# Kernel tuning notes

Hardware: AMD Instinct MI355X
Metric: run time of the kernel (lower is better)

The kernel has to match this reference:

```python
import jax, jax.numpy as jnp
import numpy as np

CLAMP = 1e20
EPS_LN = 1e-5
EPS_DEN = 1e-5


def setup_inputs() -> dict:
    key = jax.random.key(0)
    ks = jax.random.split(key, 8)
    B, T, Fin, D = 4, 2048, 512, 128
    s = 1.0 / np.sqrt(Fin)
    s2 = 1.0 / np.sqrt(D)
    return {
        "history": jax.random.normal(ks[0], (B, T, Fin), dtype=jnp.float32),
        "S0": jnp.zeros((B, 1, D, D), dtype=jnp.float32),
        "Z0": jnp.zeros((B, 1, D), dtype=jnp.float32),
        "Wk": jax.random.normal(ks[1], (Fin, D), dtype=jnp.float32) * s,
        "Wq": jax.random.normal(ks[2], (Fin, D), dtype=jnp.float32) * s,
        "Wv": jax.random.normal(ks[3], (Fin, D), dtype=jnp.float32) * s,
        "ln_g": jnp.ones((Fin,), dtype=jnp.float32),
        "ln_b": jnp.zeros((Fin,), dtype=jnp.float32),
        "w1": jax.random.normal(ks[4], (D, D), dtype=jnp.float32) * s2,
        "b1": jnp.zeros((D,), dtype=jnp.float32),
        "w2": jax.random.normal(ks[5], (D, D), dtype=jnp.float32) * s2,
        "b2": jnp.zeros((D,), dtype=jnp.float32),
        "sc_w": jax.random.normal(ks[6], (Fin, D), dtype=jnp.float32) * s,
        "sc_b": jnp.zeros((D,), dtype=jnp.float32),
    }


def reference(history, S0, Z0, Wk, Wq, Wv, ln_g, ln_b, w1, b1, w2, b2, sc_w, sc_b):
    # LayerNorm over feature dim
    mu = jnp.mean(history, axis=-1, keepdims=True)
    var = jnp.mean((history - mu) ** 2, axis=-1, keepdims=True)
    x = (history - mu) / jnp.sqrt(var + EPS_LN) * ln_g + ln_b  # [B,T,Fin]

    phi = lambda z: jax.nn.elu(z) + 1.0
    K = phi(x @ Wk)  # [B,T,D]
    Q = phi(x @ Wq)  # [B,T,D]
    V = x @ Wv       # [B,T,D]

    # S_t = clamp(cumsum_t(K_t outer V_t)) + S0  -> [B,T,D,D]
    KV = jnp.einsum('bti,btj->btij', K, V)
    S = jnp.clip(jnp.cumsum(KV, axis=1), -CLAMP, CLAMP) + S0
    # Z_t = clamp(cumsum_t(K_t)) + Z0 -> [B,T,D]
    Z = jnp.clip(jnp.cumsum(K, axis=1), -CLAMP, CLAMP) + Z0

    numerator = jnp.einsum('bti,btil->btl', Q, S)            # [B,T,D]
    denominator = jnp.einsum('bti,bti->bt', Q, Z)[..., None] + EPS_DEN
    out = numerator / denominator

    # feed-forward: Linear->ReLU->Linear->ReLU
    out = jax.nn.relu(jax.nn.relu(out @ w1 + b1) @ w2 + b2)
    # residual shortcut from normalized input
    out = out + x @ sc_w + sc_b
    return out, S, Z
```

## Files before the change

kernel.cpp:

```cpp
#include <hip/hip_runtime.h>
#include <math.h>

#define BB 4
#define TT 2048
#define FIN 512
#define DD 128
#define NC 64
#define CT 32
#define ROWS (BB*TT)
#define CLAMP_V 1e20f
#define EPS_LN_ 1e-5f
#define EPS_DEN_ 1e-5f

__global__ __launch_bounds__(256) void k0_stats(const float* __restrict__ h,
                                                float* __restrict__ stats) {
  int wv = threadIdx.x >> 6, lane = threadIdx.x & 63;
  int row = blockIdx.x * 4 + wv;
  const float* hr = h + (size_t)row * FIN;
  float s = 0.f, sq = 0.f;
#pragma unroll
  for (int j = 0; j < FIN / 64; ++j) {
    float v = hr[lane + 64 * j];
    s += v; sq += v * v;
  }
#pragma unroll
  for (int m = 32; m >= 1; m >>= 1) {
    s += __shfl_xor(s, m);
    sq += __shfl_xor(sq, m);
  }
  if (lane == 0) {
    float mu = s * (1.f / FIN);
    float var = sq * (1.f / FIN) - mu * mu;
    stats[row * 2] = mu;
    stats[row * 2 + 1] = rsqrtf(var + EPS_LN_);
  }
}

__global__ __launch_bounds__(256) void k1_lngemm(
    const float* __restrict__ h, const float* __restrict__ stats,
    const float* __restrict__ ln_g, const float* __restrict__ ln_b,
    const float* __restrict__ Wk, const float* __restrict__ Wq,
    const float* __restrict__ Wv, const float* __restrict__ Wsc,
    float* __restrict__ Kb, float* __restrict__ Qb,
    float* __restrict__ Vb, float* __restrict__ SCb) {
  __shared__ float As[32 * 129];
  __shared__ float Bs[32 * 128];
  __shared__ float stS[256];
  __shared__ float lnS[2 * FIN];
  int tid = threadIdx.x;
  int row0 = blockIdx.x * 128;
  int wsel = blockIdx.y;
  const float* W = (wsel == 0) ? Wk : (wsel == 1) ? Wq : (wsel == 2) ? Wv : Wsc;
  float* Ob = (wsel == 0) ? Kb : (wsel == 1) ? Qb : (wsel == 2) ? Vb : SCb;
  int ty = tid >> 4, tx = tid & 15;
  if (tid < 128) {
    stS[tid * 2] = stats[(row0 + tid) * 2];
    stS[tid * 2 + 1] = stats[(row0 + tid) * 2 + 1];
  }
  for (int j = tid; j < FIN; j += 256) {
    lnS[j] = ln_g[j];
    lnS[FIN + j] = ln_b[j];
  }
  float acc[8][8];
#pragma unroll
  for (int i = 0; i < 8; ++i)
#pragma unroll
    for (int j = 0; j < 8; ++j) acc[i][j] = 0.f;

  int ar = tid >> 5, af = tid & 31;
  int bk = tid >> 7, bn = tid & 127;
  float ra[16], rb[16];
#pragma unroll
  for (int j = 0; j < 16; ++j) {
    ra[j] = h[(size_t)(row0 + ar + 8 * j) * FIN + af];
    rb[j] = W[(size_t)(bk + 2 * j) * DD + bn];
  }
  __syncthreads();
#pragma unroll
  for (int j = 0; j < 16; ++j) {
    int r = ar + 8 * j;
    float mu = stS[r * 2], rs = stS[r * 2 + 1];
    As[af * 129 + r] = (ra[j] - mu) * rs * lnS[af] + lnS[FIN + af];
    Bs[(bk + 2 * j) * 128 + bn] = rb[j];
  }
  __syncthreads();

  for (int ks = 0; ks < FIN; ks += 32) {
    bool more = (ks + 32) < FIN;
    if (more) {
#pragma unroll
      for (int j = 0; j < 16; ++j) {
        ra[j] = h[(size_t)(row0 + ar + 8 * j) * FIN + ks + 32 + af];
        rb[j] = W[(size_t)(ks + 32 + bk + 2 * j) * DD + bn];
      }
    }
#pragma unroll
    for (int k = 0; k < 32; ++k) {
      float a[8], bv[8];
#pragma unroll
      for (int i = 0; i < 8; ++i) a[i] = As[k * 129 + ty * 8 + i];
#pragma unroll
      for (int j = 0; j < 8; ++j) bv[j] = Bs[k * 128 + tx * 8 + j];
#pragma unroll
      for (int i = 0; i < 8; ++i)
#pragma unroll
        for (int j = 0; j < 8; ++j) acc[i][j] = fmaf(a[i], bv[j], acc[i][j]);
    }
    __syncthreads();
    if (more) {
#pragma unroll
      for (int j = 0; j < 16; ++j) {
        int r = ar + 8 * j;
        float mu = stS[r * 2], rs = stS[r * 2 + 1];
        As[af * 129 + r] = (ra[j] - mu) * rs * lnS[ks + 32 + af] + lnS[FIN + ks + 32 + af];
        Bs[(bk + 2 * j) * 128 + bn] = rb[j];
      }
      __syncthreads();
    }
  }
  bool phi = (wsel < 2);
#pragma unroll
  for (int i = 0; i < 8; ++i) {
    int row = row0 + ty * 8 + i;
#pragma unroll
    for (int j = 0; j < 8; ++j) {
      float z = acc[i][j];
      if (phi) z = (z > 0.f) ? (z + 1.f) : expf(z);
      Ob[(size_t)row * DD + tx * 8 + j] = z;
    }
  }
}

__global__ __launch_bounds__(256) void k2_chunksum(const float* __restrict__ Kb,
                                                   const float* __restrict__ Vb,
                                                   float* __restrict__ kvsum,
                                                   float* __restrict__ ksum) {
  int bc = blockIdx.x;
  int b = bc >> 6, c = bc & 63;
  __shared__ float Kc[CT * 128];
  __shared__ float Vc[CT * 128];
  int tid = threadIdx.x;
  size_t base = (size_t)(b * TT + c * CT) * 128;
#pragma unroll
  for (int j = 0; j < 16; ++j) {
    int idx = tid + 256 * j;
    Kc[idx] = Kb[base + idx];
    Vc[idx] = Vb[base + idx];
  }
  __syncthreads();
  int ti = tid >> 4, tl = tid & 15;
  int i0 = ti * 8, l0 = tl * 8;
  float acc[8][8];
#pragma unroll
  for (int i = 0; i < 8; ++i)
#pragma unroll
    for (int j = 0; j < 8; ++j) acc[i][j] = 0.f;
  for (int t = 0; t < CT; ++t) {
    float kk[8], vv[8];
#pragma unroll
    for (int i = 0; i < 8; ++i) kk[i] = Kc[t * 128 + i0 + i];
#pragma unroll
    for (int j = 0; j < 8; ++j) vv[j] = Vc[t * 128 + l0 + j];
#pragma unroll
    for (int i = 0; i < 8; ++i)
#pragma unroll
      for (int j = 0; j < 8; ++j) acc[i][j] = fmaf(kk[i], vv[j], acc[i][j]);
  }
  size_t ob = (size_t)bc * 16384;
#pragma unroll
  for (int i = 0; i < 8; ++i)
#pragma unroll
    for (int j = 0; j < 8; ++j)
      kvsum[ob + (size_t)(i0 + i) * 128 + l0 + j] = acc[i][j];
  if (tid < 128) {
    float s = 0.f;
    for (int t = 0; t < CT; ++t) s += Kc[t * 128 + tid];
    ksum[bc * 128 + tid] = s;
  }
}

__global__ __launch_bounds__(256) void k3_prefix(float* __restrict__ kvsum,
                                                 float* __restrict__ ksum) {
  int gid = blockIdx.x * 256 + threadIdx.x;
  int b = gid >> 14, rem = gid & 16383;
  size_t base = (size_t)b * NC * 16384 + rem;
  float run = 0.f;
  for (int c = 0; c < NC; ++c) {
    size_t idx = base + (size_t)c * 16384;
    float t = kvsum[idx];
    kvsum[idx] = run;
    run += t;
  }
  if (gid < BB * 128) {
    int b2 = gid >> 7, i = gid & 127;
    float r2 = 0.f;
    for (int c = 0; c < NC; ++c) {
      int idx = (b2 * NC + c) * 128 + i;
      float t = ksum[idx];
      ksum[idx] = r2;
      r2 += t;
    }
  }
}

__global__ __launch_bounds__(128) void k4_zden(const float* __restrict__ Kb,
                                               const float* __restrict__ Qb,
                                               const float* __restrict__ ksum,
                                               const float* __restrict__ Z0,
                                               float* __restrict__ Zout,
                                               float* __restrict__ den) {
  __shared__ float denp[2 * CT];
  int bx = blockIdx.x;
  int b = bx >> 6, c = bx & 63;
  int i = threadIdx.x;
  int wv = i >> 6, lane = i & 63;
  float z = ksum[(b * NC + c) * 128 + i];
  float z0 = Z0[b * 128 + i];
  size_t rb = (size_t)(b * TT + c * CT) * 128;
  float kcur = Kb[rb + i], qcur = Qb[rb + i];
  for (int t = 0; t < CT; ++t) {
    float kn = 0.f, qn = 0.f;
    if (t + 1 < CT) {
      kn = Kb[rb + (size_t)(t + 1) * 128 + i];
      qn = Qb[rb + (size_t)(t + 1) * 128 + i];
    }
    z += kcur;
    float zc = fminf(fmaxf(z, -CLAMP_V), CLAMP_V) + z0;
    Zout[rb + (size_t)t * 128 + i] = zc;
    float p = qcur * zc;
#pragma unroll
    for (int m = 32; m >= 1; m >>= 1) p += __shfl_xor(p, m);
    if (lane == 0) denp[wv * CT + t] = p;
    kcur = kn; qcur = qn;
  }
  __syncthreads();
  if (i < CT) den[b * TT + c * CT + i] = denp[i] + denp[CT + i] + EPS_DEN_;
}

__global__ __launch_bounds__(256) void k6_main(
    const float* __restrict__ Kb, const float* __restrict__ Qb,
    const float* __restrict__ Vb, const float* __restrict__ kvpref,
    const float* __restrict__ S0, const float* __restrict__ den,
    float* __restrict__ Sout, float* __restrict__ Aout) {
  __shared__ float KQ[CT * 128 * 2];
  __shared__ float NA[4 * CT * 64];
  int tid = threadIdx.x;
  int lhalf = blockIdx.x, c = blockIdx.y, b = blockIdx.z;
  int w = tid >> 6, lane = tid & 63;
  int i0 = w * 32;
  int l = lhalf * 64 + lane;
  int row0r = b * TT + c * CT;
  size_t rowbase = (size_t)row0r * 128;
#pragma unroll
  for (int j = 0; j < 16; ++j) {
    int idx = tid + 256 * j;
    KQ[idx * 2] = Kb[rowbase + idx];
    KQ[idx * 2 + 1] = Qb[rowbase + idx];
  }
  float s[32], s0[32];
  int bc = b * NC + c;
#pragma unroll
  for (int ii = 0; ii < 32; ++ii) {
    s[ii] = kvpref[(size_t)bc * 16384 + (size_t)(i0 + ii) * 128 + l];
    s0[ii] = S0[((size_t)b * 128 + i0 + ii) * 128 + l];
  }
  __syncthreads();
  float v = Vb[rowbase + l];
  for (int t = 0; t < CT; ++t) {
    float vn = 0.f;
    if (t + 1 < CT) vn = Vb[rowbase + (size_t)(t + 1) * 128 + l];
    float num = 0.f;
    size_t sb = ((size_t)(row0r + t) * 128 + i0) * 128 + l;
#pragma unroll
    for (int ii = 0; ii < 32; ++ii) {
      float2 kq = *(const float2*)&KQ[(t * 128 + i0 + ii) * 2];
      s[ii] = fmaf(kq.x, v, s[ii]);
      float sc = fminf(fmaxf(s[ii], -CLAMP_V), CLAMP_V) + s0[ii];
      __builtin_nontemporal_store(sc, &Sout[sb + (size_t)ii * 128]);
      num = fmaf(kq.y, sc, num);
    }
    NA[(w * CT + t) * 64 + lane] = num;
    v = vn;
  }
  __syncthreads();
#pragma unroll
  for (int j = 0; j < 8; ++j) {
    int idx = tid + 256 * j;
    int t = idx >> 6, ll = idx & 63;
    int row = row0r + t;
    float sum = NA[idx] + NA[CT * 64 + idx] + NA[2 * CT * 64 + idx] +
                NA[3 * CT * 64 + idx];
    Aout[(size_t)row * 128 + lhalf * 64 + ll] = sum / den[row];
  }
}

__global__ __launch_bounds__(256) void k7_ff(
    const float* __restrict__ A,
    const float* __restrict__ w1, const float* __restrict__ b1,
    const float* __restrict__ w2, const float* __restrict__ b2,
    const float* __restrict__ SCb, const float* __restrict__ sc_b,
    float* __restrict__ out) {
  __shared__ float a[32 * 128];
  __shared__ float h1[32 * 128];
  int tid = threadIdx.x;
  int row0 = blockIdx.x * 32;
#pragma unroll
  for (int j = 0; j < 16; ++j) {
    int idx = tid + 256 * j;
    a[idx] = A[(size_t)(row0 + (idx >> 7)) * 128 + (idx & 127)];
  }
  __syncthreads();
  int l = tid & 127, half = tid >> 7;
  for (int rc = 0; rc < 2; ++rc) {
    int r0 = half * 16 + rc * 8;
    float acc[8];
#pragma unroll
    for (int rr = 0; rr < 8; ++rr) acc[rr] = b1[l];
    for (int k = 0; k < 128; ++k) {
      float wv = w1[k * 128 + l];
#pragma unroll
      for (int rr = 0; rr < 8; ++rr) acc[rr] = fmaf(a[(r0 + rr) * 128 + k], wv, acc[rr]);
    }
#pragma unroll
    for (int rr = 0; rr < 8; ++rr) h1[(r0 + rr) * 128 + l] = fmaxf(acc[rr], 0.f);
  }
  __syncthreads();
  for (int rc = 0; rc < 2; ++rc) {
    int r0 = half * 16 + rc * 8;
    float acc[8];
#pragma unroll
    for (int rr = 0; rr < 8; ++rr) acc[rr] = b2[l];
    for (int k = 0; k < 128; ++k) {
      float wv = w2[k * 128 + l];
#pragma unroll
      for (int rr = 0; rr < 8; ++rr) acc[rr] = fmaf(h1[(r0 + rr) * 128 + k], wv, acc[rr]);
    }
#pragma unroll
    for (int rr = 0; rr < 8; ++rr) {
      int row = row0 + r0 + rr;
      out[(size_t)row * 128 + l] =
          fmaxf(acc[rr], 0.f) + SCb[(size_t)row * 128 + l] + sc_b[l];
    }
  }
}

extern "C" void kernel_launch(void* const* d_in, const int* in_sizes, int n_in,
                              void* d_out, int out_size, void* d_ws, size_t ws_size,
                              hipStream_t stream) {
  const float* history = (const float*)d_in[0];
  const float* S0   = (const float*)d_in[1];
  const float* Z0   = (const float*)d_in[2];
  const float* Wk   = (const float*)d_in[3];
  const float* Wq   = (const float*)d_in[4];
  const float* Wv   = (const float*)d_in[5];
  const float* ln_g = (const float*)d_in[6];
  const float* ln_b = (const float*)d_in[7];
  const float* w1   = (const float*)d_in[8];
  const float* b1   = (const float*)d_in[9];
  const float* w2   = (const float*)d_in[10];
  const float* b2   = (const float*)d_in[11];
  const float* sc_w = (const float*)d_in[12];
  const float* sc_b = (const float*)d_in[13];

  float* out  = (float*)d_out;
  float* Sout = out + (size_t)ROWS * DD;
  float* Zout = Sout + (size_t)ROWS * DD * DD;

  float* ws = (float*)d_ws;
  float* stats = ws;
  float* Kb    = stats + 16384;
  float* Qb    = Kb + (size_t)ROWS * DD;
  float* Vb    = Qb + (size_t)ROWS * DD;
  float* SCb   = Vb + (size_t)ROWS * DD;
  float* kvsum = SCb + (size_t)ROWS * DD;
  float* ksum  = kvsum + (size_t)BB * NC * 16384;
  float* A     = ksum + (size_t)BB * NC * 128;
  float* den   = A + (size_t)ROWS * DD;

  k0_stats<<<ROWS / 4, 256, 0, stream>>>(history, stats);
  k1_lngemm<<<dim3(ROWS / 128, 4), 256, 0, stream>>>(history, stats, ln_g, ln_b,
                                                     Wk, Wq, Wv, sc_w,
                                                     Kb, Qb, Vb, SCb);
  k2_chunksum<<<BB * NC, 256, 0, stream>>>(Kb, Vb, kvsum, ksum);
  k3_prefix<<<(BB * DD * DD) / 256, 256, 0, stream>>>(kvsum, ksum);
  k4_zden<<<BB * NC, 128, 0, stream>>>(Kb, Qb, ksum, Z0, Zout, den);
  k6_main<<<dim3(2, NC, BB), 256, 0, stream>>>(Kb, Qb, Vb, kvsum, S0, den, Sout, A);
  k7_ff<<<ROWS / 32, 256, 0, stream>>>(A, w1, b1, w2, b2, SCb, sc_b, out);
}
```

Before: 739.3 us.

## Vectorize global loads and stores with float4 across kernels and retile FF

Converts scalar global loads and stores to float4 in the stats, LN-GEMM, chunk-sum, main and feed-forward kernels. It batches the prefix-scan loads in groups of eight and uses a nontemporal store for Z. The k6 K/Q interleaved shared buffer is split into separate arrays. The FF kernel is retiled to 4x4 per-thread outputs with vectorized weight loads. The goal is fewer memory instructions and better coalescing. The dominant cost is likely the S output store, which this leaves unchanged, so the overall effect may be small.

```diff
diff --git a/kernel.cpp b/kernel.cpp
--- a/kernel.cpp
+++ b/kernel.cpp
@@ -16,12 +16,13 @@
                                                 float* __restrict__ stats) {
   int wv = threadIdx.x >> 6, lane = threadIdx.x & 63;
   int row = blockIdx.x * 4 + wv;
-  const float* hr = h + (size_t)row * FIN;
+  const float4* hr = (const float4*)(h + (size_t)row * FIN);
   float s = 0.f, sq = 0.f;
 #pragma unroll
-  for (int j = 0; j < FIN / 64; ++j) {
-    float v = hr[lane + 64 * j];
-    s += v; sq += v * v;
+  for (int j = 0; j < 2; ++j) {
+    float4 v = hr[lane + 64 * j];
+    s += v.x + v.y + v.z + v.w;
+    sq += v.x * v.x + v.y * v.y + v.z * v.z + v.w * v.w;
   }
 #pragma unroll
   for (int m = 32; m >= 1; m >>= 1) {
@@ -67,21 +68,26 @@
 #pragma unroll
     for (int j = 0; j < 8; ++j) acc[i][j] = 0.f;
 
-  int ar = tid >> 5, af = tid & 31;
-  int bk = tid >> 7, bn = tid & 127;
-  float ra[16], rb[16];
-#pragma unroll
-  for (int j = 0; j < 16; ++j) {
-    ra[j] = h[(size_t)(row0 + ar + 8 * j) * FIN + af];
-    rb[j] = W[(size_t)(bk + 2 * j) * DD + bn];
-  }
-  __syncthreads();
-#pragma unroll
-  for (int j = 0; j < 16; ++j) {
-    int r = ar + 8 * j;
+  int ar = tid >> 3;
+  int af = (tid & 7) * 4;
+  int bk = tid >> 5;
+  int bn = (tid & 31) * 4;
+  float4 ra[4], rb[4];
+#pragma unroll
+  for (int p = 0; p < 4; ++p) {
+    ra[p] = *(const float4*)&h[(size_t)(row0 + ar + 32 * p) * FIN + af];
+    rb[p] = *(const float4*)&W[(size_t)(bk + 8 * p) * DD + bn];
+  }
+  __syncthreads();
+#pragma unroll
+  for (int p = 0; p < 4; ++p) {
+    int r = ar + 32 * p;
     float mu = stS[r * 2], rs = stS[r * 2 + 1];
-    As[af * 129 + r] = (ra[j] - mu) * rs * lnS[af] + lnS[FIN + af];
-    Bs[(bk + 2 * j) * 128 + bn] = rb[j];
+    As[(af + 0) * 129 + r] = (ra[p].x - mu) * rs * lnS[af + 0] + lnS[FIN + af + 0];
+    As[(af + 1) * 129 + r] = (ra[p].y - mu) * rs * lnS[af + 1] + lnS[FIN + af + 1];
+    As[(af + 2) * 129 + r] = (ra[p].z - mu) * rs * lnS[af + 2] + lnS[FIN + af + 2];
+    As[(af + 3) * 129 + r] = (ra[p].w - mu) * rs * lnS[af + 3] + lnS[FIN + af + 3];
+    *(float4*)&Bs[(bk + 8 * p) * 128 + bn] = rb[p];
   }
   __syncthreads();
 
@@ -89,9 +95,9 @@
     bool more = (ks + 32) < FIN;
     if (more) {
 #pragma unroll
-      for (int j = 0; j < 16; ++j) {
-        ra[j] = h[(size_t)(row0 + ar + 8 * j) * FIN + ks + 32 + af];
-        rb[j] = W[(size_t)(ks + 32 + bk + 2 * j) * DD + bn];
+      for (int p = 0; p < 4; ++p) {
+        ra[p] = *(const float4*)&h[(size_t)(row0 + ar + 32 * p) * FIN + ks + 32 + af];
+        rb[p] = *(const float4*)&W[(size_t)(ks + 32 + bk + 8 * p) * DD + bn];
       }
     }
 #pragma unroll
@@ -109,11 +115,15 @@
     __syncthreads();
     if (more) {
 #pragma unroll
-      for (int j = 0; j < 16; ++j) {
-        int r = ar + 8 * j;
+      for (int p = 0; p < 4; ++p) {
+        int r = ar + 32 * p;
         float mu = stS[r * 2], rs = stS[r * 2 + 1];
-        As[af * 129 + r] = (ra[j] - mu) * rs * lnS[ks + 32 + af] + lnS[FIN + ks + 32 + af];
-        Bs[(bk + 2 * j) * 128 + bn] = rb[j];
+        int f = ks + 32 + af;
+        As[(af + 0) * 129 + r] = (ra[p].x - mu) * rs * lnS[f + 0] + lnS[FIN + f + 0];
+        As[(af + 1) * 129 + r] = (ra[p].y - mu) * rs * lnS[f + 1] + lnS[FIN + f + 1];
+        As[(af + 2) * 129 + r] = (ra[p].z - mu) * rs * lnS[f + 2] + lnS[FIN + f + 2];
+        As[(af + 3) * 129 + r] = (ra[p].w - mu) * rs * lnS[f + 3] + lnS[FIN + f + 3];
+        *(float4*)&Bs[(bk + 8 * p) * 128 + bn] = rb[p];
       }
       __syncthreads();
     }
@@ -122,12 +132,16 @@
 #pragma unroll
   for (int i = 0; i < 8; ++i) {
     int row = row0 + ty * 8 + i;
-#pragma unroll
-    for (int j = 0; j < 8; ++j) {
-      float z = acc[i][j];
-      if (phi) z = (z > 0.f) ? (z + 1.f) : expf(z);
-      Ob[(size_t)row * DD + tx * 8 + j] = z;
-    }
+    float4 o0, o1;
+    float* z = &acc[i][0];
+    if (phi) {
+#pragma unroll
+      for (int j = 0; j < 8; ++j) z[j] = (z[j] > 0.f) ? (z[j] + 1.f) : expf(z[j]);
+    }
+    o0.x = z[0]; o0.y = z[1]; o0.z = z[2]; o0.w = z[3];
+    o1.x = z[4]; o1.y = z[5]; o1.z = z[6]; o1.w = z[7];
+    *(float4*)&Ob[(size_t)row * DD + tx * 8] = o0;
+    *(float4*)&Ob[(size_t)row * DD + tx * 8 + 4] = o1;
   }
 }
 
@@ -142,10 +156,10 @@
   int tid = threadIdx.x;
   size_t base = (size_t)(b * TT + c * CT) * 128;
 #pragma unroll
-  for (int j = 0; j < 16; ++j) {
-    int idx = tid + 256 * j;
-    Kc[idx] = Kb[base + idx];
-    Vc[idx] = Vb[base + idx];
+  for (int j = 0; j < 4; ++j) {
+    int i4 = tid + 256 * j;
+    *(float4*)&Kc[i4 * 4] = *(const float4*)&Kb[base + (size_t)i4 * 4];
+    *(float4*)&Vc[i4 * 4] = *(const float4*)&Vb[base + (size_t)i4 * 4];
   }
   __syncthreads();
   int ti = tid >> 4, tl = tid & 15;
@@ -170,8 +184,9 @@
 #pragma unroll
   for (int i = 0; i < 8; ++i)
 #pragma unroll
-    for (int j = 0; j < 8; ++j)
-      kvsum[ob + (size_t)(i0 + i) * 128 + l0 + j] = acc[i][j];
+    for (int j = 0; j < 8; j += 4)
+      *(float4*)&kvsum[ob + (size_t)(i0 + i) * 128 + l0 + j] =
+          make_float4(acc[i][j], acc[i][j + 1], acc[i][j + 2], acc[i][j + 3]);
   if (tid < 128) {
     float s = 0.f;
     for (int t = 0; t < CT; ++t) s += Kc[t * 128 + tid];
@@ -185,20 +200,28 @@
   int b = gid >> 14, rem = gid & 16383;
   size_t base = (size_t)b * NC * 16384 + rem;
   float run = 0.f;
-  for (int c = 0; c < NC; ++c) {
-    size_t idx = base + (size_t)c * 16384;
-    float t = kvsum[idx];
-    kvsum[idx] = run;
-    run += t;
+  for (int g = 0; g < NC; g += 8) {
+    float v[8];
+#pragma unroll
+    for (int j = 0; j < 8; ++j) v[j] = kvsum[base + (size_t)(g + j) * 16384];
+#pragma unroll
+    for (int j = 0; j < 8; ++j) {
+      kvsum[base + (size_t)(g + j) * 16384] = run;
+      run += v[j];
+    }
   }
   if (gid < BB * 128) {
     int b2 = gid >> 7, i = gid & 127;
     float r2 = 0.f;
-    for (int c = 0; c < NC; ++c) {
-      int idx = (b2 * NC + c) * 128 + i;
-      float t = ksum[idx];
-      ksum[idx] = r2;
-      r2 += t;
+    for (int g = 0; g < NC; g += 8) {
+      float v[8];
+#pragma unroll
+      for (int j = 0; j < 8; ++j) v[j] = ksum[(b2 * NC + g + j) * 128 + i];
+#pragma unroll
+      for (int j = 0; j < 8; ++j) {
+        ksum[(b2 * NC + g + j) * 128 + i] = r2;
+        r2 += v[j];
+      }
     }
   }
 }
@@ -226,7 +249,7 @@
     }
     z += kcur;
     float zc = fminf(fmaxf(z, -CLAMP_V), CLAMP_V) + z0;
-    Zout[rb + (size_t)t * 128 + i] = zc;
+    __builtin_nontemporal_store(zc, &Zout[rb + (size_t)t * 128 + i]);
     float p = qcur * zc;
 #pragma unroll
     for (int m = 32; m >= 1; m >>= 1) p += __shfl_xor(p, m);
@@ -242,7 +265,8 @@
     const float* __restrict__ Vb, const float* __restrict__ kvpref,
     const float* __restrict__ S0, const float* __restrict__ den,
     float* __restrict__ Sout, float* __restrict__ Aout) {
-  __shared__ float KQ[CT * 128 * 2];
+  __shared__ float Ks[CT * 128];
+  __shared__ float Qs[CT * 128];
   __shared__ float NA[4 * CT * 64];
   int tid = threadIdx.x;
   int lhalf = blockIdx.x, c = blockIdx.y, b = blockIdx.z;
@@ -252,10 +276,10 @@
   int row0r = b * TT + c * CT;
   size_t rowbase = (size_t)row0r * 128;
 #pragma unroll
-  for (int j = 0; j < 16; ++j) {
-    int idx = tid + 256 * j;
-    KQ[idx * 2] = Kb[rowbase + idx];
-    KQ[idx * 2 + 1] = Qb[rowbase + idx];
+  for (int j = 0; j < 4; ++j) {
+    int i4 = tid + 256 * j;
+    *(float4*)&Ks[i4 * 4] = *(const float4*)&Kb[rowbase + (size_t)i4 * 4];
+    *(float4*)&Qs[i4 * 4] = *(const float4*)&Qb[rowbase + (size_t)i4 * 4];
   }
   float s[32], s0[32];
   int bc = b * NC + c;
@@ -273,11 +297,12 @@
     size_t sb = ((size_t)(row0r + t) * 128 + i0) * 128 + l;
 #pragma unroll
     for (int ii = 0; ii < 32; ++ii) {
-      float2 kq = *(const float2*)&KQ[(t * 128 + i0 + ii) * 2];
-      s[ii] = fmaf(kq.x, v, s[ii]);
+      float kk = Ks[t * 128 + i0 + ii];
+      float qq = Qs[t * 128 + i0 + ii];
+      s[ii] = fmaf(kk, v, s[ii]);
       float sc = fminf(fmaxf(s[ii], -CLAMP_V), CLAMP_V) + s0[ii];
       __builtin_nontemporal_store(sc, &Sout[sb + (size_t)ii * 128]);
-      num = fmaf(kq.y, sc, num);
+      num = fmaf(qq, sc, num);
     }
     NA[(w * CT + t) * 64 + lane] = num;
     v = vn;
@@ -305,42 +330,69 @@
   int tid = threadIdx.x;
   int row0 = blockIdx.x * 32;
 #pragma unroll
-  for (int j = 0; j < 16; ++j) {
-    int idx = tid + 256 * j;
-    a[idx] = A[(size_t)(row0 + (idx >> 7)) * 128 + (idx & 127)];
-  }
-  __syncthreads();
-  int l = tid & 127, half = tid >> 7;
-  for (int rc = 0; rc < 2; ++rc) {
-    int r0 = half * 16 + rc * 8;
-    float acc[8];
-#pragma unroll
-    for (int rr = 0; rr < 8; ++rr) acc[rr] = b1[l];
-    for (int k = 0; k < 128; ++k) {
-      float wv = w1[k * 128 + l];
-#pragma unroll
-      for (int rr = 0; rr < 8; ++rr) acc[rr] = fmaf(a[(r0 + rr) * 128 + k], wv, acc[rr]);
-    }
-#pragma unroll
-    for (int rr = 0; rr < 8; ++rr) h1[(r0 + rr) * 128 + l] = fmaxf(acc[rr], 0.f);
-  }
-  __syncthreads();
-  for (int rc = 0; rc < 2; ++rc) {
-    int r0 = half * 16 + rc * 8;
-    float acc[8];
-#pragma unroll
-    for (int rr = 0; rr < 8; ++rr) acc[rr] = b2[l];
-    for (int k = 0; k < 128; ++k) {
-      float wv = w2[k * 128 + l];
-#pragma unroll
-      for (int rr = 0; rr < 8; ++rr) acc[rr] = fmaf(h1[(r0 + rr) * 128 + k], wv, acc[rr]);
-    }
-#pragma unroll
-    for (int rr = 0; rr < 8; ++rr) {
-      int row = row0 + r0 + rr;
-      out[(size_t)row * 128 + l] =
-          fmaxf(acc[rr], 0.f) + SCb[(size_t)row * 128 + l] + sc_b[l];
-    }
+  for (int j = 0; j < 4; ++j) {
+    int i4 = tid + 256 * j;
+    *(float4*)&a[i4 * 4] = *(const float4*)&A[(size_t)row0 * 128 + (size_t)i4 * 4];
+  }
+  __syncthreads();
+  int tx = tid & 31, ty = tid >> 5;
+  int l0 = tx * 4, r0 = ty * 4;
+  float acc[4][4];
+  float4 bb = *(const float4*)&b1[l0];
+#pragma unroll
+  for (int r = 0; r < 4; ++r) {
+    acc[r][0] = bb.x; acc[r][1] = bb.y; acc[r][2] = bb.z; acc[r][3] = bb.w;
+  }
+  for (int k = 0; k < 128; ++k) {
+    float4 wv = *(const float4*)&w1[k * 128 + l0];
+    float av[4];
+#pragma unroll
+    for (int r = 0; r < 4; ++r) av[r] = a[(r0 + r) * 128 + k];
+#pragma unroll
+    for (int r = 0; r < 4; ++r) {
+      acc[r][0] = fmaf(av[r], wv.x, acc[r][0]);
+      acc[r][1] = fmaf(av[r], wv.y, acc[r][1]);
+      acc[r][2] = fmaf(av[r], wv.z, acc[r][2]);
+      acc[r][3] = fmaf(av[r], wv.w, acc[r][3]);
+    }
+  }
+#pragma unroll
+  for (int r = 0; r < 4; ++r) {
+    float4 o;
+    o.x = fmaxf(acc[r][0], 0.f); o.y = fmaxf(acc[r][1], 0.f);
+    o.z = fmaxf(acc[r][2], 0.f); o.w = fmaxf(acc[r][3], 0.f);
+    *(float4*)&h1[(r0 + r) * 128 + l0] = o;
+  }
+  __syncthreads();
+  bb = *(const float4*)&b2[l0];
+#pragma unroll
+  for (int r = 0; r < 4; ++r) {
+    acc[r][0] = bb.x; acc[r][1] = bb.y; acc[r][2] = bb.z; acc[r][3] = bb.w;
+  }
+  for (int k = 0; k < 128; ++k) {
+    float4 wv = *(const float4*)&w2[k * 128 + l0];
+    float av[4];
+#pragma unroll
+    for (int r = 0; r < 4; ++r) av[r] = h1[(r0 + r) * 128 + k];
+#pragma unroll
+    for (int r = 0; r < 4; ++r) {
+      acc[r][0] = fmaf(av[r], wv.x, acc[r][0]);
+      acc[r][1] = fmaf(av[r], wv.y, acc[r][1]);
+      acc[r][2] = fmaf(av[r], wv.z, acc[r][2]);
+      acc[r][3] = fmaf(av[r], wv.w, acc[r][3]);
+    }
+  }
+  float4 scb = *(const float4*)&sc_b[l0];
+#pragma unroll
+  for (int r = 0; r < 4; ++r) {
+    int row = row0 + r0 + r;
+    float4 sc = *(const float4*)&SCb[(size_t)row * 128 + l0];
+    float4 o;
+    o.x = fmaxf(acc[r][0], 0.f) + sc.x + scb.x;
+    o.y = fmaxf(acc[r][1], 0.f) + sc.y + scb.y;
+    o.z = fmaxf(acc[r][2], 0.f) + sc.z + scb.z;
+    o.w = fmaxf(acc[r][3], 0.f) + sc.w + scb.w;
+    *(float4*)&out[(size_t)row * 128 + l0] = o;
   }
 }
 
```

Measured after the change: 723.4 us. 2.2% less time.
